# Kernel tuning notes

Hardware: AMD Instinct MI355X
Metric: run time of the kernel (lower is better)

## Reference

```python
import jax, jax.numpy as jnp
import numpy as np

DIM, H, HD = 1024, 16, 64

def setup_inputs() -> dict:
    key = jax.random.key(0)
    ks = jax.random.split(key, 9)
    s = 1.0 / np.sqrt(DIM)
    return {
        "x": jax.random.normal(ks[0], (4, 4096, DIM), dtype=jnp.float32),
        "time_mix": jnp.ones((1, 1, DIM), dtype=jnp.float32),
        "time_decay": jnp.ones((H, HD), dtype=jnp.float32),
        "time_first": jnp.zeros((H, HD), dtype=jnp.float32),
        "Wk": jax.random.uniform(ks[1], (DIM, DIM), jnp.float32, -s, s),
        "Wv": jax.random.uniform(ks[2], (DIM, DIM), jnp.float32, -s, s),
        "Wr": jax.random.uniform(ks[3], (DIM, DIM), jnp.float32, -s, s),
        "Wg": jax.random.uniform(ks[4], (DIM, DIM), jnp.float32, -s, s),
        "Wo": jax.random.uniform(ks[5], (DIM, DIM), jnp.float32, -s, s),
    }

def reference(x, time_mix, time_decay, time_first, Wk, Wv, Wr, Wg, Wo):
    B, T, D = x.shape
    xx = time_mix * x
    # torch Linear: y = x @ W.T
    def proj(W):
        return jnp.einsum('btd,ed->bte', xx, W).reshape(B, T, H, HD)
    k = proj(Wk)
    v = proj(Wv)
    r = proj(Wr)
    g = jax.nn.silu(proj(Wg))
    decay = jnp.exp(-time_decay)[None, :, :, None]        # [1,H,K,1]
    tf = time_first[None]                                  # [1,H,K]
    state0 = jnp.zeros((B, H, HD, HD), dtype=x.dtype)      # [B,H,K,V]

    def step(state, inp):
        k_t, v_t, r_t, g_t = inp                           # each [B,H,K]
        state = state * decay + k_t[..., :, None] * v_t[..., None, :]
        wkv = jnp.einsum('bhkv,bhk->bhv', state, k_t) + tf * k_t * v_t
        return state, r_t * wkv * g_t

    # time-major for scan: [T,B,H,K]
    tm = lambda a: jnp.moveaxis(a, 1, 0)
    state, outs = jax.lax.scan(step, state0, (tm(k), tm(v), tm(r), tm(g)))
    out = jnp.moveaxis(outs, 0, 1).reshape(B, T, D)        # [B,T,D]
    out = jnp.einsum('btd,ed->bte', out, Wo)
    return out, state
```

## Files before the change

kernel.cpp:

```cpp
#include <hip/hip_runtime.h>
#include <stdint.h>

#define DIM 1024
#define NH  16
#define HD  64
#define BB  4
#define TT  4096
#define BT  (BB*TT)
#define NC  32
#define CL  128

typedef __bf16 bf16x8 __attribute__((ext_vector_type(8)));
typedef float  f32x4  __attribute__((ext_vector_type(4)));

__device__ __forceinline__ float bfu(unsigned int u) {
    return __uint_as_float((u & 0xffffu) << 16);
}
__device__ __forceinline__ unsigned short f2bf(float f) {
    unsigned int u = __float_as_uint(f);
    u += 0x7fffu + ((u >> 16) & 1u);
    return (unsigned short)(u >> 16);
}

__device__ __forceinline__ void gload16(const void* g, void* lds) {
    __builtin_amdgcn_global_load_lds((__attribute__((address_space(1))) void*)g,
                                     (__attribute__((address_space(3))) void*)lds,
                                     16, 0, 0);
}


__global__ __launch_bounds__(256) void conv_x_kernel(
    const float* __restrict__ x, const float* __restrict__ tmix,
    unsigned short* __restrict__ xx)
{
    int gid = blockIdx.x * 256 + threadIdx.x;
    float4 xv = ((const float4*)x)[gid];
    float4 tv = ((const float4*)tmix)[gid & 255];
    uint2 o;
    o.x = (unsigned)f2bf(xv.x * tv.x) | ((unsigned)f2bf(xv.y * tv.y) << 16);
    o.y = (unsigned)f2bf(xv.z * tv.z) | ((unsigned)f2bf(xv.w * tv.w) << 16);
    ((uint2*)xx)[gid] = o;
}

__global__ __launch_bounds__(256) void conv_w_kernel(
    const float* __restrict__ Wk, const float* __restrict__ Wv,
    const float* __restrict__ Wr, const float* __restrict__ Wg,
    const float* __restrict__ Wo,
    unsigned short* __restrict__ wcat, unsigned short* __restrict__ wob)
{
    int gid = blockIdx.x * 256 + threadIdx.x;
    size_t idx = (size_t)gid * 4;
    float4 v;
    unsigned short* dst;
    if (idx < 4194304) {
        int p = (int)(idx >> 20);
        size_t loc = idx & 1048575;
        const float* src = (p == 0) ? Wk : (p == 1) ? Wv : (p == 2) ? Wr : Wg;
        v = ((const float4*)src)[loc >> 2];
        dst = wcat + idx;
    } else {
        size_t loc = idx - 4194304;
        v = ((const float4*)Wo)[loc >> 2];
        dst = wob + loc;
    }
    uint2 o;
    o.x = (unsigned)f2bf(v.x) | ((unsigned)f2bf(v.y) << 16);
    o.y = (unsigned)f2bf(v.z) | ((unsigned)f2bf(v.w) << 16);
    *(uint2*)dst = o;
}

__global__ __launch_bounds__(256) void rg_merge(
    unsigned short* __restrict__ rb, const unsigned short* __restrict__ gb)
{
    int gid = blockIdx.x * 256 + threadIdx.x;
    uint2 rv = ((const uint2*)rb)[gid];
    uint2 gv = ((const uint2*)gb)[gid];
    uint2 o;
    o.x = (unsigned)f2bf(bfu(rv.x) * bfu(gv.x)) |
          ((unsigned)f2bf(bfu(rv.x >> 16) * bfu(gv.x >> 16)) << 16);
    o.y = (unsigned)f2bf(bfu(rv.y) * bfu(gv.y)) |
          ((unsigned)f2bf(bfu(rv.y >> 16) * bfu(gv.y >> 16)) << 16);
    ((uint2*)rb)[gid] = o;
}


#define MFMAQ(accb, av, bv)                                                    \
    _Pragma("unroll") for (int mi_ = 0; mi_ < 4; ++mi_)                        \
    _Pragma("unroll") for (int ni_ = 0; ni_ < 4; ++ni_)                        \
        acc[(accb)+mi_][ni_] = __builtin_amdgcn_mfma_f32_16x16x32_bf16(        \
            av[mi_], bv[ni_], acc[(accb)+mi_][ni_], 0, 0, 0);

#define LDA4(dst, mib, kh, bi)                                                 \
    _Pragma("unroll") for (int q_ = 0; q_ < 4; ++q_)                           \
        dst[q_] = *(const bf16x8*)&As[bi][(kh)*8192 + (arow + ((mib)+q_)*16)*32 + kxu];

#define LDB4(dst, kh, bi)                                                      \
    _Pragma("unroll") for (int q_ = 0; q_ < 4; ++q_)                           \
        dst[q_] = *(const bf16x8*)&Bs[bi][(kh)*8192 + (brow + q_*16)*32 + kxu];

#define STAGE_A(nb, kh, k0e) do {                                              \
    gload16(Asrc0 + (k0e) + (kh)*32, &As[nb][(kh)*8192 + d0]);                 \
    gload16(Asrc1 + (k0e) + (kh)*32, &As[nb][(kh)*8192 + d1]); } while (0)

#define STAGE_B(nb, kh, k0e) do {                                              \
    gload16(Bsrc0 + (k0e) + (kh)*32, &Bs[nb][(kh)*8192 + d0]);                 \
    gload16(Bsrc1 + (k0e) + (kh)*32, &Bs[nb][(kh)*8192 + d1]); } while (0)

#define SBAR()  __builtin_amdgcn_s_barrier()
#define SCHED0() __builtin_amdgcn_sched_barrier(0)
#define WAIT_LGKM0() asm volatile("s_waitcnt lgkmcnt(0)" ::: "memory")
#define WAIT_VM(n)   asm volatile("s_waitcnt vmcnt(" #n ")" ::: "memory")

template<int EPI>
__global__ __launch_bounds__(512, 2) void gemm256(
    const unsigned short* __restrict__ A, const unsigned short* __restrict__ B,
    float* __restrict__ C, int M, int N, int K,
    unsigned short* __restrict__ kb, unsigned short* __restrict__ vb,
    unsigned short* __restrict__ rb, unsigned short* __restrict__ gb)
{
    __shared__ unsigned short As[2][16384];
    __shared__ unsigned short Bs[2][16384];

    const int tid  = threadIdx.x;
    const int lane = tid & 63;
    const int wv   = tid >> 6;
    const int wr   = wv >> 2;
    const int wc   = wv & 3;
    const int lrow = lane & 15;
    const int kseg = lane >> 4;

    const int nwg = gridDim.x;
    const int cpx = nwg >> 3;
    const int bid = blockIdx.x;
    const int wg  = (bid & 7) * cpx + (bid >> 3);
    const int nbx = N >> 8;
    const int bx = wg % nbx, by = wg / nbx;
    const size_t bm = (size_t)by * 256, bn = (size_t)bx * 256;

    const int r0 = tid >> 2;
    const int c0 = (tid & 3) ^ (((tid >> 5) & 1) << 1);
    const int r1 = (512 + tid) >> 2;
    const int c1 = (tid & 3) ^ ((((512 + tid) >> 5) & 1) << 1);
    const unsigned short* Asrc0 = A + (bm + r0) * (size_t)K + c0 * 8;
    const unsigned short* Asrc1 = A + (bm + r1) * (size_t)K + c1 * 8;
    const unsigned short* Bsrc0 = B + (bn + r0) * (size_t)K + c0 * 8;
    const unsigned short* Bsrc1 = B + (bn + r1) * (size_t)K + c1 * 8;
    const int d0 = (tid & 448) * 8;
    const int d1 = (512 + (tid & 448)) * 8;

    const int arow = wr * 128 + lrow;
    const int brow = wc * 64 + lrow;
    const int kxu  = ((kseg * 16) ^ ((lrow >> 3) << 5)) >> 1;

    f32x4 acc[8][4] = {};
    bf16x8 aP[4], aQ[4], bP[4], bQ[4];
    const int NT = K >> 6;

    STAGE_A(0, 0, 0); STAGE_B(0, 0, 0); STAGE_A(0, 1, 0); STAGE_B(0, 1, 0);
    WAIT_VM(4);
    SBAR(); SCHED0();
    LDA4(aP, 0, 0, 0);
    LDB4(bP, 0, 0);
    SCHED0();

    for (int t = 0; t < NT; ++t) {
        const int bufc = t & 1, bufn = bufc ^ 1;
        const int k0n = (t + 1) << 6;
        const bool more = (t + 1 < NT);
        SBAR();
        WAIT_LGKM0(); SCHED0();
        if (more) STAGE_A(bufn, 0, k0n);
        __builtin_amdgcn_s_setprio(1);
        MFMAQ(0, aP, bP);
        __builtin_amdgcn_s_setprio(0);
        LDA4(aQ, 4, 0, bufc);
        SCHED0();
        WAIT_VM(2);
        SBAR();
        WAIT_LGKM0(); SCHED0();
        if (more) STAGE_B(bufn, 0, k0n);
        __builtin_amdgcn_s_setprio(1);
        MFMAQ(4, aQ, bP);
        __builtin_amdgcn_s_setprio(0);
        LDA4(aP, 0, 1, bufc);
        LDB4(bQ, 1, bufc);
        SCHED0();
        SBAR();
        WAIT_LGKM0(); SCHED0();
        if (more) STAGE_A(bufn, 1, k0n);
        __builtin_amdgcn_s_setprio(1);
        MFMAQ(0, aP, bQ);
        __builtin_amdgcn_s_setprio(0);
        LDA4(aQ, 4, 1, bufc);
        SCHED0();
        WAIT_VM(2);
        SBAR();
        WAIT_LGKM0(); SCHED0();
        if (more) STAGE_B(bufn, 1, k0n);
        __builtin_amdgcn_s_setprio(1);
        MFMAQ(4, aQ, bQ);
        __builtin_amdgcn_s_setprio(0);
        if (more) {
            LDA4(aP, 0, 0, bufn);
            LDB4(bP, 0, bufn);
        }
        SCHED0();
    }

    if (EPI == 0) {
        const int p = (int)(bn >> 10);
        unsigned short* dst = (p == 0) ? kb : (p == 1) ? vb : (p == 2) ? rb : gb;
        #pragma unroll
        for (int mi = 0; mi < 8; ++mi) {
            const int mbase = (int)bm + wr * 128 + mi * 16 + kseg * 4;
            #pragma unroll
            for (int ni = 0; ni < 4; ++ni) {
                const int n = (int)bn + wc * 64 + ni * 16 + lrow;
                const int e = n & 1023;
                const int h = e >> 6, j = e & 63;
                #pragma unroll
                for (int ri = 0; ri < 4; ++ri) {
                    const int m = mbase + ri;
                    const int b = m >> 12, tt = m & 4095;
                    float v = acc[mi][ni][ri];
                    if (p == 3) v = v / (1.f + __expf(-v));
                    dst[(((size_t)(b * NH + h)) * TT + tt) * HD + j] = f2bf(v);
                }
            }
        }
    } else {
        #pragma unroll
        for (int mi = 0; mi < 8; ++mi) {
            const int mbase = (int)bm + wr * 128 + mi * 16 + kseg * 4;
            #pragma unroll
            for (int ni = 0; ni < 4; ++ni) {
                const int n = (int)bn + wc * 64 + ni * 16 + lrow;
                #pragma unroll
                for (int ri = 0; ri < 4; ++ri)
                    C[(size_t)(mbase + ri) * N + n] = acc[mi][ni][ri];
            }
        }
    }
}


__global__ __launch_bounds__(256) void chunk_fused(
    const unsigned short* __restrict__ kb, const unsigned short* __restrict__ vb,
    const unsigned short* __restrict__ rgb,
    const float* __restrict__ td, const float* __restrict__ tf,
    float* __restrict__ contrib, unsigned short* __restrict__ outp)
{
    __shared__ unsigned short KS [128 * 64];
    __shared__ unsigned short VT [64 * 128];
    __shared__ unsigned short Qm [32 * 64];
    __shared__ unsigned short QDm[32 * 64];
    __shared__ unsigned short KTB[32 * 64];
    __shared__ unsigned short KDT[64 * 32];
    __shared__ unsigned short PMt[32 * 32];
    __shared__ unsigned short SPT[64 * 64];

    const int bid  = blockIdx.x;
    const int c    = bid & (NC - 1);
    const int bh   = bid >> 5;
    const int h    = bh & (NH - 1);
    const int batch= bh >> 4;
    const int tid  = threadIdx.x;
    const int lane = tid & 63;
    const int w    = tid >> 6;
    const int lrow = lane & 15;
    const int kseg = lane >> 4;

    const float* tdh = td + h * HD;

    const unsigned short* kg_ = kb + ((size_t)bh * TT + (size_t)c * CL) * HD;
    const unsigned short* vg_ = vb + ((size_t)bh * TT + (size_t)c * CL) * HD;
    ((uint4*)KS)[tid]       = ((const uint4*)kg_)[tid];
    ((uint4*)KS)[tid + 256] = ((const uint4*)kg_)[tid + 256];
    ((uint4*)KS)[tid + 512] = ((const uint4*)kg_)[tid + 512];
    ((uint4*)KS)[tid + 768] = ((const uint4*)kg_)[tid + 768];
    #pragma unroll
    for (int it = 0; it < 4; ++it) {
        int ci = it * 256 + tid;
        uint4 r = ((const uint4*)vg_)[ci];
        int s = ci >> 3, j0 = (ci & 7) * 8;
        unsigned int vals[4] = { r.x, r.y, r.z, r.w };
        #pragma unroll
        for (int q = 0; q < 4; ++q) {
            int j1 = j0 + 2 * q, j2 = j1 + 1;
            *(unsigned short*)((char*)VT + ((j1 * 256 + s * 2) ^ ((j1 & 15) << 4)))
                = (unsigned short)(vals[q] & 0xffffu);
            *(unsigned short*)((char*)VT + ((j2 * 256 + s * 2) ^ ((j2 & 15) << 4)))
                = (unsigned short)(vals[q] >> 16);
        }
    }

    const int kkc = tid & 63;
    const float t1 = tdh[kkc];

    float e32[4];
    #pragma unroll
    for (int q = 0; q < 4; ++q)
        e32[q] = __expf(-32.f * tdh[16 * w + kseg * 4 + q]);

    const int it = w >> 1;
    const int st = w & 1;
    const int jt0 = (w & 1) * 2;

    f32x4 acc_S[4] = {};

    for (int sb = 0; sb < 4; ++sb) {
        const int s0 = sb * 32;
        __syncthreads();
        #pragma unroll
        for (int i8 = 0; i8 < 8; ++i8) {
            int r = i8 * 4 + w;
            float kf  = bfu(KS[(s0 + r) * 64 + kkc]);
            float eq  = __expf(-t1 * (float)r);
            float eq1 = __expf(-t1 * (float)(r + 1));
            float ek  = __expf( t1 * (float)r);
            float ekd = __expf(-t1 * (float)(31 - r));
            int rb2 = (r * 128 + kkc * 2) ^ ((r & 7) << 4);
            *(unsigned short*)((char*)Qm  + rb2) = f2bf(kf * eq);
            *(unsigned short*)((char*)QDm + rb2) = f2bf(kf * eq1);
            *(unsigned short*)((char*)KTB + rb2) = f2bf(kf * ek);
            *(unsigned short*)((char*)KDT + ((kkc * 64 + r * 2) ^ ((kkc & 3) << 4)))
                = f2bf(kf * ekd);
        }
        __syncthreads();
        {
            bf16x8 qa[2], kbf[2];
            #pragma unroll
            for (int ks = 0; ks < 2; ++ks) {
                qa[ks] = *(const bf16x8*)((const char*)Qm +
                    (it * 16 + lrow) * 128 + ((kseg * 16 + ks * 64) ^ ((lrow & 7) << 4)));
                kbf[ks] = *(const bf16x8*)((const char*)KTB +
                    (st * 16 + lrow) * 128 + ((kseg * 16 + ks * 64) ^ ((lrow & 7) << 4)));
            }
            f32x4 accP = {};
            accP = __builtin_amdgcn_mfma_f32_16x16x32_bf16(qa[0], kbf[0], accP, 0, 0, 0);
            accP = __builtin_amdgcn_mfma_f32_16x16x32_bf16(qa[1], kbf[1], accP, 0, 0, 0);
            #pragma unroll
            for (int q = 0; q < 4; ++q) {
                int i_ = it * 16 + kseg * 4 + q;
                int s_ = st * 16 + lrow;
                unsigned short pv = (s_ <= i_) ? f2bf(accP[q]) : (unsigned short)0;
                *(unsigned short*)((char*)PMt + ((i_ * 64 + s_ * 2) ^ ((i_ & 3) << 4))) = pv;
            }
        }
        {
            bf16x8 sa = *(const bf16x8*)((const char*)KDT +
                (16 * w + lrow) * 64 + ((kseg * 16) ^ ((lrow & 3) << 4)));
            #pragma unroll
            for (int jt = 0; jt < 4; ++jt) {
                #pragma unroll
                for (int q = 0; q < 4; ++q) acc_S[jt][q] *= e32[q];
                bf16x8 vbf = *(const bf16x8*)((const char*)VT +
                    (jt * 16 + lrow) * 256 + ((s0 * 2 + kseg * 16) ^ ((lrow & 15) << 4)));
                acc_S[jt] = __builtin_amdgcn_mfma_f32_16x16x32_bf16(sa, vbf, acc_S[jt], 0, 0, 0);
            }
        }
        __syncthreads();
        {
            bf16x8 pa = *(const bf16x8*)((const char*)PMt +
                (it * 16 + lrow) * 64 + ((kseg * 16) ^ ((lrow & 3) << 4)));
            bf16x8 qd[2];
            #pragma unroll
            for (int ks = 0; ks < 2; ++ks)
                qd[ks] = *(const bf16x8*)((const char*)QDm +
                    (it * 16 + lrow) * 128 + ((kseg * 16 + ks * 64) ^ ((lrow & 7) << 4)));
            #pragma unroll
            for (int jj = 0; jj < 2; ++jj) {
                const int jt = jt0 + jj;
                const int j_ = jt * 16 + lrow;
                bf16x8 vbf = *(const bf16x8*)((const char*)VT +
                    j_ * 256 + ((s0 * 2 + kseg * 16) ^ ((lrow & 15) << 4)));
                f32x4 accO = {};
                accO = __builtin_amdgcn_mfma_f32_16x16x32_bf16(pa, vbf, accO, 0, 0, 0);
                if (sb > 0) {
                    #pragma unroll
                    for (int ks = 0; ks < 2; ++ks) {
                        bf16x8 sp = *(const bf16x8*)((const char*)SPT +
                            j_ * 128 + ((kseg * 16 + ks * 64) ^ ((lrow & 7) << 4)));
                        accO = __builtin_amdgcn_mfma_f32_16x16x32_bf16(qd[ks], sp, accO, 0, 0, 0);
                    }
                }
                const float tfj = tf[h * HD + j_];
                #pragma unroll
                for (int q = 0; q < 4; ++q) {
                    int ip = it * 16 + kseg * 4 + q;
                    int t_ = c * CL + s0 + ip;
                    float kval = bfu(KS[(s0 + ip) * 64 + j_]);
                    float vval = bfu(*(const unsigned short*)((const char*)VT +
                        j_ * 256 + (((s0 + ip) * 2) ^ ((j_ & 15) << 4))));
                    float val = accO[q] + tfj * kval * vval;
                    float rgv = bfu(rgb[((size_t)bh * TT + t_) * HD + j_]);
                    outp[((size_t)batch * TT + t_) * DIM + h * HD + j_] = f2bf(val * rgv);
                }
            }
        }
        __syncthreads();
        if (sb < 3) {
            #pragma unroll
            for (int jt = 0; jt < 4; ++jt) {
                const int j_ = jt * 16 + lrow;
                #pragma unroll
                for (int q = 0; q < 4; ++q) {
                    int kk_ = 16 * w + kseg * 4 + q;
                    *(unsigned short*)((char*)SPT +
                        ((j_ * 128 + kk_ * 2) ^ ((j_ & 7) << 4))) = f2bf(acc_S[jt][q]);
                }
            }
        }
    }

    float* cb = contrib + (size_t)bid * 4096;
    #pragma unroll
    for (int jt = 0; jt < 4; ++jt) {
        const int j_ = jt * 16 + lrow;
        *(f32x4*)&cb[j_ * 64 + 16 * w + kseg * 4] = acc_S[jt];
    }
}


__global__ __launch_bounds__(256) void chunk_scan(
    const float* __restrict__ contrib, const float* __restrict__ td,
    unsigned short* __restrict__ s0t, float* __restrict__ state_out)
{
    int gtid = blockIdx.x * 256 + threadIdx.x;
    int kk = gtid & 63;
    int j  = (gtid >> 6) & 63;
    int bh = gtid >> 12;
    int h  = bh & (NH - 1);
    float dC = __expf(-(float)CL * td[h * HD + kk]);
    float S = 0.f;
    const float* base = contrib + ((size_t)bh * NC) * 4096 + j * 64 + kk;
    unsigned short* sb = s0t + ((size_t)bh * NC) * 4096 + j * 64 + kk;
    for (int c = 0; c < NC; c++) {
        sb[(size_t)c * 4096] = f2bf(S);
        S = __builtin_fmaf(dC, S, base[(size_t)c * 4096]);
    }
    state_out[(size_t)bh * 4096 + kk * 64 + j] = S;
}


__global__ __launch_bounds__(256) void chunk_corr(
    const unsigned short* __restrict__ kb, const unsigned short* __restrict__ rgb,
    const float* __restrict__ td, const unsigned short* __restrict__ s0t,
    unsigned short* __restrict__ outp)
{
    const int bid = blockIdx.x;
    const int c   = bid & (NC - 1);
    const int bh  = bid >> 5;
    const int h   = bh & (NH - 1);
    const int b   = bh >> 4;
    const int tid = threadIdx.x;
    const int lane = tid & 63;
    const int w    = tid >> 6;

    __shared__ unsigned short kd[CL * HD];

    const int srow = tid >> 3;
    const int kk0  = (tid & 7) * 8;
    float tdv[8];
    #pragma unroll
    for (int e = 0; e < 8; e++) tdv[e] = td[h * HD + kk0 + e];
    const unsigned short* kbase = kb + ((size_t)bh * TT + (size_t)c * CL) * HD;
    #pragma unroll
    for (int it = 0; it < 4; it++) {
        const int row = it * 32 + srow;
        uint4 r = *(const uint4*)(kbase + (size_t)row * HD + kk0);
        const float fi = -(float)(row + 1);
        unsigned int rr[4] = { r.x, r.y, r.z, r.w };
        unsigned int o[4];
        #pragma unroll
        for (int q = 0; q < 4; q++) {
            float lo = bfu(rr[q])       * __expf(fi * tdv[2*q]);
            float hi = bfu(rr[q] >> 16) * __expf(fi * tdv[2*q+1]);
            o[q] = (unsigned)f2bf(lo) | ((unsigned)f2bf(hi) << 16);
        }
        *(uint4*)((char*)kd + row * 128 + ((kk0 * 2) ^ ((row & 7) << 4))) =
            make_uint4(o[0], o[1], o[2], o[3]);
    }
    __syncthreads();

    const int lrow = lane & 15;
    const int g    = lane >> 4;

    bf16x8 afr[2][4], bfr[2][2];
    const unsigned short* sbase = s0t + (size_t)bid * 4096;
    #pragma unroll
    for (int ks = 0; ks < 2; ks++)
        #pragma unroll
        for (int vt = 0; vt < 4; vt++)
            afr[ks][vt] = *(const bf16x8*)(sbase + (vt * 16 + lrow) * 64 + g * 8 + ks * 32);
    #pragma unroll
    for (int ks = 0; ks < 2; ks++)
        #pragma unroll
        for (int bt = 0; bt < 2; bt++) {
            const int row = w * 32 + bt * 16 + lrow;
            bfr[ks][bt] = *(const bf16x8*)((const char*)kd + row * 128 +
                (((g * 8 + ks * 32) * 2) ^ ((row & 7) << 4)));
        }

    f32x4 acc[4][2] = {};
    #pragma unroll
    for (int ks = 0; ks < 2; ks++)
        #pragma unroll
        for (int vt = 0; vt < 4; vt++)
            #pragma unroll
            for (int bt = 0; bt < 2; bt++)
                acc[vt][bt] = __builtin_amdgcn_mfma_f32_16x16x32_bf16(
                    afr[ks][vt], bfr[ks][bt], acc[vt][bt], 0, 0, 0);

    #pragma unroll
    for (int bt = 0; bt < 2; bt++) {
        const int i = w * 32 + bt * 16 + lrow;
        const size_t t = (size_t)c * CL + i;
        const unsigned short* rgrow = rgb + ((size_t)bh * TT + t) * HD;
        unsigned short* orow = outp + ((size_t)b * TT + t) * DIM + h * HD;
        #pragma unroll
        for (int vt = 0; vt < 4; vt++)
            #pragma unroll
            for (int ri = 0; ri < 4; ri++) {
                const int v = vt * 16 + 4 * g + ri;
                float val = bfu(orow[v]) + bfu(rgrow[v]) * acc[vt][bt][ri];
                orow[v] = f2bf(val);
            }
    }
}


static const size_t OFF_XX   = 0;
static const size_t OFF_WCAT = 33554432;
static const size_t OFF_WO   = 41943040;
static const size_t OFF_K    = 44040192;
static const size_t OFF_V    = 77594624;
static const size_t OFF_R    = 111149056;
static const size_t OFF_G    = 144703488;
static const size_t OFF_OP   = 0;

extern "C" void kernel_launch(void* const* d_in, const int* in_sizes, int n_in,
                              void* d_out, int out_size, void* d_ws, size_t ws_size,
                              hipStream_t stream) {
    const float* x   = (const float*)d_in[0];
    const float* tmx = (const float*)d_in[1];
    const float* td  = (const float*)d_in[2];
    const float* tf  = (const float*)d_in[3];
    const float* Wk  = (const float*)d_in[4];
    const float* Wv  = (const float*)d_in[5];
    const float* Wr  = (const float*)d_in[6];
    const float* Wg  = (const float*)d_in[7];
    const float* Wo  = (const float*)d_in[8];

    char* ws = (char*)d_ws;
    unsigned short* xx   = (unsigned short*)(ws + OFF_XX);
    unsigned short* wcat = (unsigned short*)(ws + OFF_WCAT);
    unsigned short* wob  = (unsigned short*)(ws + OFF_WO);
    unsigned short* kb   = (unsigned short*)(ws + OFF_K);
    unsigned short* vb   = (unsigned short*)(ws + OFF_V);
    unsigned short* rb   = (unsigned short*)(ws + OFF_R);
    unsigned short* gb   = (unsigned short*)(ws + OFF_G);
    float*          ctr  = (float*)(ws + OFF_G);
    unsigned short* s0t  = (unsigned short*)(ws + OFF_V);
    unsigned short* outp = (unsigned short*)(ws + OFF_OP);

    float* out       = (float*)d_out;
    float* state_out = out + (size_t)BT * DIM;

    conv_x_kernel<<<16384, 256, 0, stream>>>(x, tmx, xx);
    conv_w_kernel<<<5120, 256, 0, stream>>>(Wk, Wv, Wr, Wg, Wo, wcat, wob);
    gemm256<0><<<1024, 512, 0, stream>>>(xx, wcat, nullptr,
                                         BT, 4096, 1024, kb, vb, rb, gb);
    rg_merge<<<16384, 256, 0, stream>>>(rb, gb);
    chunk_fused<<<64 * NC, 256, 0, stream>>>(kb, vb, rb, td, tf, ctr, outp);
    chunk_scan<<<1024, 256, 0, stream>>>(ctr, td, s0t, state_out);
    chunk_corr<<<64 * NC, 256, 0, stream>>>(kb, rb, td, s0t, outp);
    gemm256<1><<<256, 512, 0, stream>>>(outp, wob, out,
                                        BT, 1024, 1024,
                                        nullptr, nullptr, nullptr, nullptr);
}
```

Measured before the change: 338.9 us.

## Fuse r*g into consumers, persistent projection GEMM with LDS-staged epilogue, bf16 chunk states

Drops the separate rg_merge kernel; the chunk kernels now multiply r and g on the fly. The projection GEMM becomes persistent: 256 blocks each handle four tiles, prefetching the next tile's first K stage during the epilogue. Output is staged through LDS so head-major stores are coalesced 16-byte writes. Chunk contributions are stored as bf16 and the scan updates them in place, halving that traffic at some precision cost.

```diff
diff --git a/kernel.cpp b/kernel.cpp
--- a/kernel.cpp
+++ b/kernel.cpp
@@ -69,20 +69,6 @@
     *(uint2*)dst = o;
 }
 
-__global__ __launch_bounds__(256) void rg_merge(
-    unsigned short* __restrict__ rb, const unsigned short* __restrict__ gb)
-{
-    int gid = blockIdx.x * 256 + threadIdx.x;
-    uint2 rv = ((const uint2*)rb)[gid];
-    uint2 gv = ((const uint2*)gb)[gid];
-    uint2 o;
-    o.x = (unsigned)f2bf(bfu(rv.x) * bfu(gv.x)) |
-          ((unsigned)f2bf(bfu(rv.x >> 16) * bfu(gv.x >> 16)) << 16);
-    o.y = (unsigned)f2bf(bfu(rv.y) * bfu(gv.y)) |
-          ((unsigned)f2bf(bfu(rv.y >> 16) * bfu(gv.y >> 16)) << 16);
-    ((uint2*)rb)[gid] = o;
-}
-
 
 #define MFMAQ(accb, av, bv)                                                    \
     _Pragma("unroll") for (int mi_ = 0; mi_ < 4; ++mi_)                        \
@@ -111,12 +97,165 @@
 #define WAIT_LGKM0() asm volatile("s_waitcnt lgkmcnt(0)" ::: "memory")
 #define WAIT_VM(n)   asm volatile("s_waitcnt vmcnt(" #n ")" ::: "memory")
 
-template<int EPI>
-__global__ __launch_bounds__(512, 2) void gemm256(
+#define KLOOP_BODY()                                                           \
+    for (int t = 0; t < NT; ++t) {                                             \
+        const int bufc = t & 1, bufn = bufc ^ 1;                               \
+        const int k0n = (t + 1) << 6;                                          \
+        const bool more = (t + 1 < NT);                                        \
+        SBAR();                                                                \
+        WAIT_LGKM0(); SCHED0();                                                \
+        if (more) STAGE_A(bufn, 0, k0n);                                       \
+        __builtin_amdgcn_s_setprio(1);                                         \
+        MFMAQ(0, aP, bP);                                                      \
+        __builtin_amdgcn_s_setprio(0);                                         \
+        LDA4(aQ, 4, 0, bufc);                                                  \
+        SCHED0();                                                              \
+        WAIT_VM(2);                                                            \
+        SBAR();                                                                \
+        WAIT_LGKM0(); SCHED0();                                                \
+        if (more) STAGE_B(bufn, 0, k0n);                                       \
+        __builtin_amdgcn_s_setprio(1);                                         \
+        MFMAQ(4, aQ, bP);                                                      \
+        __builtin_amdgcn_s_setprio(0);                                         \
+        LDA4(aP, 0, 1, bufc);                                                  \
+        LDB4(bQ, 1, bufc);                                                     \
+        SCHED0();                                                              \
+        SBAR();                                                                \
+        WAIT_LGKM0(); SCHED0();                                                \
+        if (more) STAGE_A(bufn, 1, k0n);                                       \
+        __builtin_amdgcn_s_setprio(1);                                         \
+        MFMAQ(0, aP, bQ);                                                      \
+        __builtin_amdgcn_s_setprio(0);                                         \
+        LDA4(aQ, 4, 1, bufc);                                                  \
+        SCHED0();                                                              \
+        WAIT_VM(2);                                                            \
+        SBAR();                                                                \
+        WAIT_LGKM0(); SCHED0();                                                \
+        if (more) STAGE_B(bufn, 1, k0n);                                       \
+        __builtin_amdgcn_s_setprio(1);                                         \
+        MFMAQ(4, aQ, bQ);                                                      \
+        __builtin_amdgcn_s_setprio(0);                                         \
+        if (more) {                                                            \
+            LDA4(aP, 0, 0, bufn);                                              \
+            LDB4(bP, 0, bufn);                                                 \
+        }                                                                      \
+        SCHED0();                                                              \
+    }
+
+
+__global__ __launch_bounds__(512, 2) void gemm_proj(
     const unsigned short* __restrict__ A, const unsigned short* __restrict__ B,
-    float* __restrict__ C, int M, int N, int K,
     unsigned short* __restrict__ kb, unsigned short* __restrict__ vb,
     unsigned short* __restrict__ rb, unsigned short* __restrict__ gb)
+{
+    __shared__ unsigned short As[2][16384];
+    __shared__ unsigned short Bs[2][16384];
+    const int K = 1024, NT = 16;
+
+    const int tid  = threadIdx.x;
+    const int lane = tid & 63;
+    const int wv   = tid >> 6;
+    const int wr   = wv >> 2;
+    const int wc   = wv & 3;
+    const int lrow = lane & 15;
+    const int kseg = lane >> 4;
+
+    const int r0 = tid >> 2;
+    const int c0 = (tid & 3) ^ (((tid >> 5) & 1) << 1);
+    const int r1 = (512 + tid) >> 2;
+    const int c1 = (tid & 3) ^ ((((512 + tid) >> 5) & 1) << 1);
+    const int d0 = (tid & 448) * 8;
+    const int d1 = (512 + (tid & 448)) * 8;
+
+    const int arow = wr * 128 + lrow;
+    const int brow = wc * 64 + lrow;
+    const int kxu  = ((kseg * 16) ^ ((lrow >> 3) << 5)) >> 1;
+
+    const int P = blockIdx.x;
+    size_t bm = 0, bn = 0;
+    const unsigned short *Asrc0 = A, *Asrc1 = A, *Bsrc0 = B, *Bsrc1 = B;
+    auto setTile = [&](int u) {
+        int wg = (P & 7) * 128 + (P >> 3) * 4 + u;
+        bn = (size_t)(wg & 15) << 8;
+        bm = (size_t)(wg >> 4) << 8;
+        Asrc0 = A + (bm + r0) * (size_t)K + c0 * 8;
+        Asrc1 = A + (bm + r1) * (size_t)K + c1 * 8;
+        Bsrc0 = B + (bn + r0) * (size_t)K + c0 * 8;
+        Bsrc1 = B + (bn + r1) * (size_t)K + c1 * 8;
+    };
+
+    setTile(0);
+    STAGE_A(0, 0, 0); STAGE_B(0, 0, 0); STAGE_A(0, 1, 0); STAGE_B(0, 1, 0);
+
+    for (int u = 0; u < 4; ++u) {
+        const size_t bmc = bm, bnc = bn;
+        f32x4 acc[8][4] = {};
+        bf16x8 aP[4], aQ[4], bP[4], bQ[4];
+
+        if (u == 0) WAIT_VM(4); else WAIT_VM(20);
+        SBAR(); SCHED0();
+        LDA4(aP, 0, 0, 0);
+        LDB4(bP, 0, 0);
+        SCHED0();
+
+        KLOOP_BODY();
+
+        if (u < 3) {
+            setTile(u + 1);
+            STAGE_A(0, 0, 0); STAGE_B(0, 0, 0); STAGE_A(0, 1, 0); STAGE_B(0, 1, 0);
+        }
+
+        const int pidx = (int)(bnc >> 10);
+        unsigned short* dstb = (pidx == 0) ? kb : (pidx == 1) ? vb :
+                               (pidx == 2) ? rb : gb;
+        const int b_ = (int)(bmc >> 12);
+        const int h0 = (int)((bnc & 1023) >> 6);
+        const bool dosilu = (pidx == 3);
+
+        SBAR();
+        #pragma unroll
+        for (int pass = 0; pass < 2; ++pass) {
+            if ((wc >> 1) == pass) {
+                unsigned short* reg_ = (wc & 1) ? &Bs[1][0] : &As[1][0];
+                #pragma unroll
+                for (int mi = 0; mi < 8; ++mi)
+                    #pragma unroll
+                    for (int ni = 0; ni < 4; ++ni)
+                        #pragma unroll
+                        for (int ri = 0; ri < 4; ++ri) {
+                            int trow = wr * 128 + mi * 16 + kseg * 4 + ri;
+                            int j = ni * 16 + lrow;
+                            float v = acc[mi][ni][ri];
+                            if (dosilu) v = v / (1.f + __expf(-v));
+                            *(unsigned short*)((char*)reg_ +
+                                ((trow * 128 + j * 2) ^ ((trow & 7) << 4))) = f2bf(v);
+                        }
+            }
+            SBAR();
+            #pragma unroll
+            for (int half = 0; half < 2; ++half) {
+                const unsigned short* reg_ = half ? &Bs[1][0] : &As[1][0];
+                const int p = pass * 2 + half;
+                unsigned short* pb = dstb +
+                    (((size_t)(b_ * NH + h0 + p)) * TT + (bmc & 4095)) * HD;
+                #pragma unroll
+                for (int q = 0; q < 4; ++q) {
+                    int o = tid * 64 + q * 16;
+                    int trow = o >> 7;
+                    uint4 val = *(const uint4*)((const char*)reg_ +
+                                                (o ^ ((trow & 7) << 4)));
+                    *(uint4*)((char*)pb + o) = val;
+                }
+            }
+            SBAR();
+        }
+    }
+}
+
+
+__global__ __launch_bounds__(512, 2) void gemm_out(
+    const unsigned short* __restrict__ A, const unsigned short* __restrict__ B,
+    float* __restrict__ C, int M, int N, int K)
 {
     __shared__ unsigned short As[2][16384];
     __shared__ unsigned short Bs[2][16384];
@@ -163,92 +302,27 @@
     LDB4(bP, 0, 0);
     SCHED0();
 
-    for (int t = 0; t < NT; ++t) {
-        const int bufc = t & 1, bufn = bufc ^ 1;
-        const int k0n = (t + 1) << 6;
-        const bool more = (t + 1 < NT);
-        SBAR();
-        WAIT_LGKM0(); SCHED0();
-        if (more) STAGE_A(bufn, 0, k0n);
-        __builtin_amdgcn_s_setprio(1);
-        MFMAQ(0, aP, bP);
-        __builtin_amdgcn_s_setprio(0);
-        LDA4(aQ, 4, 0, bufc);
-        SCHED0();
-        WAIT_VM(2);
-        SBAR();
-        WAIT_LGKM0(); SCHED0();
-        if (more) STAGE_B(bufn, 0, k0n);
-        __builtin_amdgcn_s_setprio(1);
-        MFMAQ(4, aQ, bP);
-        __builtin_amdgcn_s_setprio(0);
-        LDA4(aP, 0, 1, bufc);
-        LDB4(bQ, 1, bufc);
-        SCHED0();
-        SBAR();
-        WAIT_LGKM0(); SCHED0();
-        if (more) STAGE_A(bufn, 1, k0n);
-        __builtin_amdgcn_s_setprio(1);
-        MFMAQ(0, aP, bQ);
-        __builtin_amdgcn_s_setprio(0);
-        LDA4(aQ, 4, 1, bufc);
-        SCHED0();
-        WAIT_VM(2);
-        SBAR();
-        WAIT_LGKM0(); SCHED0();
-        if (more) STAGE_B(bufn, 1, k0n);
-        __builtin_amdgcn_s_setprio(1);
-        MFMAQ(4, aQ, bQ);
-        __builtin_amdgcn_s_setprio(0);
-        if (more) {
-            LDA4(aP, 0, 0, bufn);
-            LDB4(bP, 0, bufn);
-        }
-        SCHED0();
-    }
-
-    if (EPI == 0) {
-        const int p = (int)(bn >> 10);
-        unsigned short* dst = (p == 0) ? kb : (p == 1) ? vb : (p == 2) ? rb : gb;
-        #pragma unroll
-        for (int mi = 0; mi < 8; ++mi) {
-            const int mbase = (int)bm + wr * 128 + mi * 16 + kseg * 4;
-            #pragma unroll
-            for (int ni = 0; ni < 4; ++ni) {
-                const int n = (int)bn + wc * 64 + ni * 16 + lrow;
-                const int e = n & 1023;
-                const int h = e >> 6, j = e & 63;
-                #pragma unroll
-                for (int ri = 0; ri < 4; ++ri) {
-                    const int m = mbase + ri;
-                    const int b = m >> 12, tt = m & 4095;
-                    float v = acc[mi][ni][ri];
-                    if (p == 3) v = v / (1.f + __expf(-v));
-                    dst[(((size_t)(b * NH + h)) * TT + tt) * HD + j] = f2bf(v);
-                }
-            }
-        }
-    } else {
-        #pragma unroll
-        for (int mi = 0; mi < 8; ++mi) {
-            const int mbase = (int)bm + wr * 128 + mi * 16 + kseg * 4;
-            #pragma unroll
-            for (int ni = 0; ni < 4; ++ni) {
-                const int n = (int)bn + wc * 64 + ni * 16 + lrow;
-                #pragma unroll
-                for (int ri = 0; ri < 4; ++ri)
-                    C[(size_t)(mbase + ri) * N + n] = acc[mi][ni][ri];
-            }
+    KLOOP_BODY();
+
+    #pragma unroll
+    for (int mi = 0; mi < 8; ++mi) {
+        const int mbase = (int)bm + wr * 128 + mi * 16 + kseg * 4;
+        #pragma unroll
+        for (int ni = 0; ni < 4; ++ni) {
+            const int n = (int)bn + wc * 64 + ni * 16 + lrow;
+            #pragma unroll
+            for (int ri = 0; ri < 4; ++ri)
+                C[(size_t)(mbase + ri) * N + n] = acc[mi][ni][ri];
         }
     }
 }
 
 
 __global__ __launch_bounds__(256) void chunk_fused(
-    const unsigned short* __restrict__ kb, const unsigned short* __restrict__ vb,
-    const unsigned short* __restrict__ rgb,
+    const unsigned short* __restrict__ kb, const unsigned short* vb,
+    const unsigned short* __restrict__ rb, const unsigned short* __restrict__ gb,
     const float* __restrict__ td, const float* __restrict__ tf,
-    float* __restrict__ contrib, unsigned short* __restrict__ outp)
+    unsigned short* ctru, unsigned short* __restrict__ outp)
 {
     __shared__ unsigned short KS [128 * 64];
     __shared__ unsigned short VT [64 * 128];
@@ -393,7 +467,8 @@
                     float vval = bfu(*(const unsigned short*)((const char*)VT +
                         j_ * 256 + (((s0 + ip) * 2) ^ ((j_ & 15) << 4))));
                     float val = accO[q] + tfj * kval * vval;
-                    float rgv = bfu(rgb[((size_t)bh * TT + t_) * HD + j_]);
+                    size_t e = ((size_t)bh * TT + t_) * HD + j_;
+                    float rgv = bfu(rb[e]) * bfu(gb[e]);
                     outp[((size_t)batch * TT + t_) * DIM + h * HD + j_] = f2bf(val * rgv);
                 }
             }
@@ -413,18 +488,21 @@
         }
     }
 
-    float* cb = contrib + (size_t)bid * 4096;
+    unsigned short* cb = ctru + (size_t)bid * 8192;
     #pragma unroll
     for (int jt = 0; jt < 4; ++jt) {
         const int j_ = jt * 16 + lrow;
-        *(f32x4*)&cb[j_ * 64 + 16 * w + kseg * 4] = acc_S[jt];
+        uint2 pk;
+        pk.x = (unsigned)f2bf(acc_S[jt][0]) | ((unsigned)f2bf(acc_S[jt][1]) << 16);
+        pk.y = (unsigned)f2bf(acc_S[jt][2]) | ((unsigned)f2bf(acc_S[jt][3]) << 16);
+        *(uint2*)&cb[j_ * 64 + 16 * w + kseg * 4] = pk;
     }
 }
 
 
 __global__ __launch_bounds__(256) void chunk_scan(
-    const float* __restrict__ contrib, const float* __restrict__ td,
-    unsigned short* __restrict__ s0t, float* __restrict__ state_out)
+    unsigned short* ctru, const float* __restrict__ td,
+    float* __restrict__ state_out)
 {
     int gtid = blockIdx.x * 256 + threadIdx.x;
     int kk = gtid & 63;
@@ -433,19 +511,20 @@
     int h  = bh & (NH - 1);
     float dC = __expf(-(float)CL * td[h * HD + kk]);
     float S = 0.f;
-    const float* base = contrib + ((size_t)bh * NC) * 4096 + j * 64 + kk;
-    unsigned short* sb = s0t + ((size_t)bh * NC) * 4096 + j * 64 + kk;
+    unsigned short* cs = ctru + (size_t)bh * NC * 8192 + j * 64 + kk;
     for (int c = 0; c < NC; c++) {
-        sb[(size_t)c * 4096] = f2bf(S);
-        S = __builtin_fmaf(dC, S, base[(size_t)c * 4096]);
+        float t = bfu(cs[(size_t)c * 8192]);
+        cs[(size_t)c * 8192] = f2bf(S);
+        S = __builtin_fmaf(dC, S, t);
     }
     state_out[(size_t)bh * 4096 + kk * 64 + j] = S;
 }
 
 
 __global__ __launch_bounds__(256) void chunk_corr(
-    const unsigned short* __restrict__ kb, const unsigned short* __restrict__ rgb,
-    const float* __restrict__ td, const unsigned short* __restrict__ s0t,
+    const unsigned short* __restrict__ kb, const unsigned short* __restrict__ rb,
+    const unsigned short* __restrict__ gb,
+    const float* __restrict__ td, const unsigned short* s0t,
     unsigned short* __restrict__ outp)
 {
     const int bid = blockIdx.x;
@@ -487,7 +566,7 @@
     const int g    = lane >> 4;
 
     bf16x8 afr[2][4], bfr[2][2];
-    const unsigned short* sbase = s0t + (size_t)bid * 4096;
+    const unsigned short* sbase = s0t + (size_t)bid * 8192;
     #pragma unroll
     for (int ks = 0; ks < 2; ks++)
         #pragma unroll
@@ -516,14 +595,16 @@
     for (int bt = 0; bt < 2; bt++) {
         const int i = w * 32 + bt * 16 + lrow;
         const size_t t = (size_t)c * CL + i;
-        const unsigned short* rgrow = rgb + ((size_t)bh * TT + t) * HD;
+        const unsigned short* rrow2 = rb + ((size_t)bh * TT + t) * HD;
+        const unsigned short* grow2 = gb + ((size_t)bh * TT + t) * HD;
         unsigned short* orow = outp + ((size_t)b * TT + t) * DIM + h * HD;
         #pragma unroll
         for (int vt = 0; vt < 4; vt++)
             #pragma unroll
             for (int ri = 0; ri < 4; ri++) {
                 const int v = vt * 16 + 4 * g + ri;
-                float val = bfu(orow[v]) + bfu(rgrow[v]) * acc[vt][bt][ri];
+                float val = bfu(orow[v]) +
+                            bfu(rrow2[v]) * bfu(grow2[v]) * acc[vt][bt][ri];
                 orow[v] = f2bf(val);
             }
     }
@@ -560,8 +641,7 @@
     unsigned short* vb   = (unsigned short*)(ws + OFF_V);
     unsigned short* rb   = (unsigned short*)(ws + OFF_R);
     unsigned short* gb   = (unsigned short*)(ws + OFF_G);
-    float*          ctr  = (float*)(ws + OFF_G);
-    unsigned short* s0t  = (unsigned short*)(ws + OFF_V);
+    unsigned short* ctru = (unsigned short*)(ws + OFF_V);
     unsigned short* outp = (unsigned short*)(ws + OFF_OP);
 
     float* out       = (float*)d_out;
@@ -569,13 +649,9 @@
 
     conv_x_kernel<<<16384, 256, 0, stream>>>(x, tmx, xx);
     conv_w_kernel<<<5120, 256, 0, stream>>>(Wk, Wv, Wr, Wg, Wo, wcat, wob);
-    gemm256<0><<<1024, 512, 0, stream>>>(xx, wcat, nullptr,
-                                         BT, 4096, 1024, kb, vb, rb, gb);
-    rg_merge<<<16384, 256, 0, stream>>>(rb, gb);
-    chunk_fused<<<64 * NC, 256, 0, stream>>>(kb, vb, rb, td, tf, ctr, outp);
-    chunk_scan<<<1024, 256, 0, stream>>>(ctr, td, s0t, state_out);
-    chunk_corr<<<64 * NC, 256, 0, stream>>>(kb, rb, td, s0t, outp);
-    gemm256<1><<<256, 512, 0, stream>>>(outp, wob, out,
-                                        BT, 1024, 1024,
-                                        nullptr, nullptr, nullptr, nullptr);
-}
+    gemm_proj<<<256, 512, 0, stream>>>(xx, wcat, kb, vb, rb, gb);
+    chunk_fused<<<64 * NC, 256, 0, stream>>>(kb, vb, rb, gb, td, tf, ctru, outp);
+    chunk_scan<<<1024, 256, 0, stream>>>(ctru, td, state_out);
+    chunk_corr<<<64 * NC, 256, 0, stream>>>(kb, rb, gb, td, ctru, outp);
+    gemm_out<<<256, 512, 0, stream>>>(outp, wob, out, BT, 1024, 1024);
+}
```

Result: slower. 611.0 us (+80.3%).
